# Kernel optimization log

Measured on AMD Instinct MI355X. Metric: run time of the kernel, lower is better.

Reference implementation:

```python
import jax, jax.numpy as jnp
import numpy as np

P = 16      # patch size
D = 768     # d_model
H = 12      # heads
L = 12      # layers
F = 3072    # d_ff
NC = 1000   # num classes
B = 32
IMG = 224
S = (IMG // P) ** 2 + 1  # 197 tokens (CLS + patches)
EPS = 1e-5


def layernorm(x, s, b):
    m = jnp.mean(x, axis=-1, keepdims=True)
    v = jnp.var(x, axis=-1, keepdims=True)
    return (x - m) * jax.lax.rsqrt(v + EPS) * s + b


def setup_inputs() -> dict:
    key = jax.random.key(0)
    ks = jax.random.split(key, 16)
    sd = 0.02
    patch_dim = P * P * 3  # 768
    inp = {
        "img": jax.random.normal(ks[0], (B, 3, IMG, IMG), jnp.float32),
        "proj_w": jax.random.normal(ks[1], (patch_dim, D), jnp.float32) * sd,
        "proj_b": jnp.zeros((D,), jnp.float32),
        "cls_token": jax.random.normal(ks[2], (1, 1, D), jnp.float32) * sd,
        "pos_emb": jax.random.normal(ks[3], (1, S, D), jnp.float32) * sd,
        # stacked per-layer params [L, ...]
        "ln1_s": jnp.ones((L, D), jnp.float32),
        "ln1_b": jnp.zeros((L, D), jnp.float32),
        "wq": jax.random.normal(ks[4], (L, D, D), jnp.float32) * sd,
        "bq": jnp.zeros((L, D), jnp.float32),
        "wk": jax.random.normal(ks[5], (L, D, D), jnp.float32) * sd,
        "bk": jnp.zeros((L, D), jnp.float32),
        "wv": jax.random.normal(ks[6], (L, D, D), jnp.float32) * sd,
        "bv": jnp.zeros((L, D), jnp.float32),
        "wo": jax.random.normal(ks[7], (L, D, D), jnp.float32) * sd,
        "bo": jnp.zeros((L, D), jnp.float32),
        "ln2_s": jnp.ones((L, D), jnp.float32),
        "ln2_b": jnp.zeros((L, D), jnp.float32),
        "w1": jax.random.normal(ks[8], (L, D, F), jnp.float32) * sd,
        "b1": jnp.zeros((L, F), jnp.float32),
        "w2": jax.random.normal(ks[9], (L, F, D), jnp.float32) * sd,
        "b2": jnp.zeros((L, D), jnp.float32),
        "fnorm_s": jnp.ones((D,), jnp.float32),
        "fnorm_b": jnp.zeros((D,), jnp.float32),
        "head_w": jax.random.normal(ks[10], (D, NC), jnp.float32) * sd,
        "head_b": jnp.zeros((NC,), jnp.float32),
    }
    return inp


def vit_forward(img, proj_w, proj_b, cls_token, pos_emb, ln1_s, ln1_b,
                wq, bq, wk, bk, wv, bv, wo, bo, ln2_s, ln2_b,
                w1, b1, w2, b2, fnorm_s, fnorm_b, head_w, head_b):
    b = img.shape[0]
    g = IMG // P
    # rearrange 'b c (h ph) (w pw) -> b (h w) (ph pw c)'
    x = img.reshape(b, 3, g, P, g, P)
    x = x.transpose(0, 2, 4, 3, 5, 1).reshape(b, g * g, P * P * 3)
    x = x @ proj_w + proj_b                      # [b, 196, D]
    cls = jnp.broadcast_to(cls_token, (b, 1, D))
    x = jnp.concatenate([cls, x], axis=1)        # [b, 197, D]
    x = x + pos_emb                              # learnable positional encoding

    dk = D // H
    scale = 1.0 / jnp.sqrt(jnp.float32(dk))

    def layer(x, p):
        (l1s, l1b, Wq, Bq, Wk, Bk, Wv, Bv, Wo, Bo,
         l2s, l2b, W1, B1, W2, B2) = p
        # pre-norm self-attention with residual
        xn = layernorm(x, l1s, l1b)
        q = (xn @ Wq + Bq).reshape(b, S, H, dk)
        k = (xn @ Wk + Bk).reshape(b, S, H, dk)
        v = (xn @ Wv + Bv).reshape(b, S, H, dk)
        scores = jnp.einsum('bqhd,bkhd->bhqk', q, k) * scale
        attn = jax.nn.softmax(scores, axis=-1)
        ao = jnp.einsum('bhqk,bkhd->bqhd', attn, v).reshape(b, S, D)
        x = x + (ao @ Wo + Bo)
        # pre-norm FFN with residual
        xn = layernorm(x, l2s, l2b)
        h = jax.nn.gelu(xn @ W1 + B1, approximate=False)
        x = x + (h @ W2 + B2)
        return x, None

    params = (ln1_s, ln1_b, wq, bq, wk, bk, wv, bv, wo, bo,
              ln2_s, ln2_b, w1, b1, w2, b2)
    x, _ = jax.lax.scan(layer, x, params)
    x = layernorm(x, fnorm_s, fnorm_b)
    cls_out = x[:, 0, :]
    return cls_out @ head_w + head_b             # [b, num_classes]


def reference(img, proj_w, proj_b, cls_token, pos_emb, ln1_s, ln1_b,
              wq, bq, wk, bk, wv, bv, wo, bo, ln2_s, ln2_b,
              w1, b1, w2, b2, fnorm_s, fnorm_b, head_w, head_b):
    return vit_forward(img, proj_w, proj_b, cls_token, pos_emb, ln1_s, ln1_b,
                       wq, bq, wk, bk, wv, bv, wo, bo, ln2_s, ln2_b,
                       w1, b1, w2, b2, fnorm_s, fnorm_b, head_w, head_b)
```

## Files before the change

kernel.cpp:

```cpp
#include <hip/hip_runtime.h>
#include <stdint.h>

typedef __attribute__((ext_vector_type(4))) float  f32x4;
typedef __attribute__((ext_vector_type(8))) _Float16 f16x8;
typedef __attribute__((ext_vector_type(8))) unsigned short u16x8;

__device__ __forceinline__ unsigned short f2h(float f) {
    _Float16 h = (_Float16)f;
    union { _Float16 h; unsigned short u; } cv; cv.h = h; return cv.u;
}

__device__ __forceinline__ f32x4 mfma16(f16x8 a, f16x8 b, f32x4 c) {
    return __builtin_amdgcn_mfma_f32_16x16x32_f16(a, b, c, 0, 0, 0);
}

__device__ __forceinline__ void async16(const unsigned short* g, unsigned short* l) {
    __builtin_amdgcn_global_load_lds(
        (const __attribute__((address_space(1))) unsigned int*)g,
        (__attribute__((address_space(3))) unsigned int*)l,
        16, 0, 0);
}

template<int EPI, int BK>
__global__ __launch_bounds__(256, (BK == 32 ? 4 : 3))
void gemm_k(const unsigned short* __restrict__ A, const unsigned short* __restrict__ Bw,
            int M, int K, int N,
            float* __restrict__ p0, unsigned short* __restrict__ p1,
            const float* __restrict__ p2, const float* __restrict__ p3,
            unsigned short* __restrict__ p4, unsigned short* __restrict__ p5)
{
    __shared__ unsigned short lA[2][64 * BK];
    __shared__ unsigned short lB[2][128 * BK];
    const int tid  = threadIdx.x;
    const int lane = tid & 63;
    const int wid  = tid >> 6;

    const int gx  = gridDim.x;
    const int nwg = gx * gridDim.y;
    const int lin = blockIdx.y * gx + blockIdx.x;
    const int q = nwg >> 3, r = nwg & 7;
    const int xcd = lin & 7, i = lin >> 3;
    const int wg  = (xcd < r ? xcd * (q + 1) : r * (q + 1) + (xcd - r) * q) + i;
    const int m0 = (wg / gx) * 64;
    const int n0 = (wg % gx) * 128;

    const int colBase = wid * 32;
    const int fr = lane & 15, fg = lane >> 4;

    f32x4 acc[4][2];
#pragma unroll
    for (int a = 0; a < 4; ++a)
#pragma unroll
        for (int b = 0; b < 2; ++b) acc[a][b] = (f32x4){0.f, 0.f, 0.f, 0.f};

    const int nk = K / BK;
    constexpr int CPR = BK / 8;
    constexpr int ACH = 64 * CPR;
    constexpr int NH  = (ACH + 128 * CPR) / 256;

    auto stage = [&](int buf, int kt) {
        const int k0 = kt * BK;
#pragma unroll
        for (int h = 0; h < NH; ++h) {
            const int c = h * 256 + tid;
            const int wbase = h * 256 + wid * 64;
            if (c < ACH) {
                const int row = c / CPR, kc = c % CPR;
                const int gkc = (BK == 32) ? (kc ^ ((row >> 1) & 3)) : (kc ^ (row & 7));
                int ar = m0 + row; if (ar > M - 1) ar = M - 1;
                async16(A + (size_t)ar * K + k0 + gkc * 8,
                        &lA[buf][(size_t)wbase * 8]);
            } else {
                const int cb = c - ACH;
                const int row = cb / CPR, kc = cb % CPR;
                const int gkc = (BK == 32) ? (kc ^ ((row >> 1) & 3)) : (kc ^ (row & 7));
                async16(Bw + (size_t)(n0 + row) * K + k0 + gkc * 8,
                        &lB[buf][(size_t)(wbase - ACH) * 8]);
            }
        }
    };

    stage(0, 0);
    for (int kt = 0; kt < nk; ++kt) {
        __syncthreads();
        if (kt + 1 < nk) stage((kt + 1) & 1, kt + 1);
        const int buf = kt & 1;
#pragma unroll
        for (int kk = 0; kk < BK / 32; ++kk) {
            f16x8 af[4], bfv[2];
#pragma unroll
            for (int mi = 0; mi < 4; ++mi) {
                int row = mi * 16 + fr;
                int pc  = (BK == 32) ? (fg ^ ((row >> 1) & 3))
                                     : ((kk * 4 + fg) ^ (row & 7));
                af[mi] = *(const f16x8*)(&lA[buf][row * BK + pc * 8]);
            }
#pragma unroll
            for (int ni = 0; ni < 2; ++ni) {
                int row = colBase + ni * 16 + fr;
                int pc  = (BK == 32) ? (fg ^ ((row >> 1) & 3))
                                     : ((kk * 4 + fg) ^ (row & 7));
                bfv[ni] = *(const f16x8*)(&lB[buf][row * BK + pc * 8]);
            }
#pragma unroll
            for (int mi = 0; mi < 4; ++mi)
#pragma unroll
                for (int ni = 0; ni < 2; ++ni)
                    acc[mi][ni] = mfma16(af[mi], bfv[ni], acc[mi][ni]);
        }
    }

#pragma unroll
    for (int mi = 0; mi < 4; ++mi) {
#pragma unroll
        for (int ni = 0; ni < 2; ++ni) {
            const int col = n0 + colBase + ni * 16 + fr;
#pragma unroll
            for (int reg = 0; reg < 4; ++reg) {
                const int row = m0 + mi * 16 + fg * 4 + reg;
                if (row >= M) continue;
                const float v = acc[mi][ni][reg];
                if constexpr (EPI == 0) {
                    int mat = col / 768;
                    int w   = col - mat * 768;
                    int h   = w >> 6, d = w & 63;
                    int b   = row / 197, s = row - b * 197;
                    float val = v + p2[col];
                    if (mat == 2) {
                        p5[(((size_t)b * 12 + h) * 64 + d) * 208 + s] = f2h(val);
                    } else {
                        unsigned short* dst = (mat == 0) ? p1 : p4;
                        dst[(((size_t)b * 12 + h) * 197 + s) * 64 + d] = f2h(val);
                    }
                } else if constexpr (EPI == 1 || EPI == 3) {
                    size_t idx = (size_t)row * 768 + col;
                    p0[idx] = p0[idx] + v + p2[col];
                } else if constexpr (EPI == 2) {
                    float val = v + p2[col];
                    float g = 0.5f * val * (1.0f + erff(val * 0.70710678118654752f));
                    p1[(size_t)row * 3072 + col] = f2h(g);
                } else {
                    int b = row / 196, p = row - b * 196;
                    float val = v + p2[col] + p3[(size_t)(1 + p) * 768 + col];
                    p0[((size_t)(b * 197 + 1 + p)) * 768 + col] = val;
                }
            }
        }
    }
}

__global__ __launch_bounds__(256, 4)
void attn_k(const unsigned short* __restrict__ qb, const unsigned short* __restrict__ kb,
            const unsigned short* __restrict__ vt, unsigned short* __restrict__ ao)
{
    __shared__ float sc[32 * 210];
    __shared__ float rinv[32];

    const int qt = blockIdx.x;
    const int bh = blockIdx.y;
    const int b = bh / 12, h = bh - b * 12;
    const unsigned short* qh  = qb + (size_t)bh * 197 * 64;
    const unsigned short* kh  = kb + (size_t)bh * 197 * 64;
    const unsigned short* vth = vt + (size_t)bh * 64 * 208;
    const int tid = threadIdx.x, lane = tid & 63, wid = tid >> 6;
    const int fr = lane & 15, fg = lane >> 4;

    f16x8 qf[2][2];
#pragma unroll
    for (int mi = 0; mi < 2; ++mi)
#pragma unroll
        for (int kc = 0; kc < 2; ++kc) {
            int s = qt * 32 + mi * 16 + fr; if (s > 196) s = 196;
            qf[mi][kc] = *(const f16x8*)(qh + (size_t)s * 64 + kc * 32 + fg * 8);
        }

    for (int nt = wid; nt < 13; nt += 4) {
        f32x4 a0 = (f32x4){0.f,0.f,0.f,0.f}, a1 = a0;
        int rs = nt * 16 + fr; if (rs > 196) rs = 196;
#pragma unroll
        for (int kc = 0; kc < 2; ++kc) {
            f16x8 kf = *(const f16x8*)(kh + (size_t)rs * 64 + kc * 32 + fg * 8);
            a0 = mfma16(qf[0][kc], kf, a0);
            a1 = mfma16(qf[1][kc], kf, a1);
        }
        int ccol = nt * 16 + fr;
        bool valid = (ccol < 197);
#pragma unroll
        for (int reg = 0; reg < 4; ++reg) {
            int mr = fg * 4 + reg;
            sc[mr * 210 + ccol]        = valid ? a0[reg] * 0.125f : -1e30f;
            sc[(16 + mr) * 210 + ccol] = valid ? a1[reg] * 0.125f : -1e30f;
        }
    }
    __syncthreads();

    {
        int row = tid >> 3, j = tid & 7;
        float m = -1e30f;
        for (int c = j; c < 208; c += 8) m = fmaxf(m, sc[row * 210 + c]);
#pragma unroll
        for (int o = 1; o < 8; o <<= 1) m = fmaxf(m, __shfl_xor(m, o));
        float sum = 0.f;
        for (int c = j; c < 208; c += 8) {
            float e = __expf(sc[row * 210 + c] - m);
            sc[row * 210 + c] = e;
            sum += e;
        }
#pragma unroll
        for (int o = 1; o < 8; o <<= 1) sum += __shfl_xor(sum, o);
        if (j == 0) rinv[row] = 1.0f / sum;
    }
    __syncthreads();

    f32x4 o0 = (f32x4){0.f,0.f,0.f,0.f}, o1 = o0;
    const int dbase = wid * 16;
    for (int kt = 0; kt < 7; ++kt) {
        int kb8 = kt * 32 + fg * 8;
        f16x8 pa0, pa1, vf;
        if (kb8 >= 208) {
#pragma unroll
            for (int j = 0; j < 8; ++j) { pa0[j] = (_Float16)0.f; pa1[j] = (_Float16)0.f; vf[j] = (_Float16)0.f; }
        } else {
            const float* pr0 = &sc[fr * 210 + kb8];
            const float* pr1 = &sc[(16 + fr) * 210 + kb8];
#pragma unroll
            for (int j = 0; j < 8; ++j) { pa0[j] = (_Float16)pr0[j]; pa1[j] = (_Float16)pr1[j]; }
            vf = *(const f16x8*)(vth + (size_t)(dbase + fr) * 208 + kb8);
        }
        o0 = mfma16(pa0, vf, o0);
        o1 = mfma16(pa1, vf, o1);
    }
#pragma unroll
    for (int reg = 0; reg < 4; ++reg) {
        int mr0 = fg * 4 + reg, s0 = qt * 32 + mr0;
        if (s0 < 197)
            ao[((size_t)(b * 197 + s0)) * 768 + h * 64 + dbase + fr] = f2h(o0[reg] * rinv[mr0]);
        int mr1 = 16 + fg * 4 + reg, s1 = qt * 32 + mr1;
        if (s1 < 197)
            ao[((size_t)(b * 197 + s1)) * 768 + h * 64 + dbase + fr] = f2h(o1[reg] * rinv[mr1]);
    }
}

__global__ __launch_bounds__(256, 4)
void ln_k(const float* __restrict__ x, const float* __restrict__ gs,
          const float* __restrict__ gb, unsigned short* __restrict__ out)
{
    const int row = blockIdx.x;
    const int tid = threadIdx.x, lane = tid & 63, wid = tid >> 6;
    const float* xr = x + (size_t)row * 768;
    float v0 = xr[tid], v1 = xr[tid + 256], v2 = xr[tid + 512];
    float s = v0 + v1 + v2;
    float q = v0 * v0 + v1 * v1 + v2 * v2;
#pragma unroll
    for (int o = 1; o < 64; o <<= 1) { s += __shfl_xor(s, o); q += __shfl_xor(q, o); }
    __shared__ float ws[4], wq[4];
    if (lane == 0) { ws[wid] = s; wq[wid] = q; }
    __syncthreads();
    s = ws[0] + ws[1] + ws[2] + ws[3];
    q = wq[0] + wq[1] + wq[2] + wq[3];
    const float mean = s * (1.0f / 768.0f);
    const float rstd = rsqrtf(q * (1.0f / 768.0f) - mean * mean + 1e-5f);
    unsigned short* orow = out + (size_t)row * 768;
    orow[tid]       = f2h((v0 - mean) * rstd * gs[tid]       + gb[tid]);
    orow[tid + 256] = f2h((v1 - mean) * rstd * gs[tid + 256] + gb[tid + 256]);
    orow[tid + 512] = f2h((v2 - mean) * rstd * gs[tid + 512] + gb[tid + 512]);
}

__device__ __forceinline__ void convT_dev(const float* __restrict__ src,
                                          unsigned short* __restrict__ dst,
                                          int K, int N, int bx, int by)
{
    __shared__ float t[64][65];
    const int tid = threadIdx.x;
    const int n0 = bx * 64, k0 = by * 64;
    int r = tid >> 4, cq = tid & 15;
#pragma unroll
    for (int i = 0; i < 4; ++i) {
        f32x4 v = *(const f32x4*)(src + (size_t)(k0 + r + i * 16) * N + n0 + cq * 4);
        t[r + i * 16][cq * 4 + 0] = v.x;
        t[r + i * 16][cq * 4 + 1] = v.y;
        t[r + i * 16][cq * 4 + 2] = v.z;
        t[r + i * 16][cq * 4 + 3] = v.w;
    }
    __syncthreads();
    int nl = tid >> 2, kq = tid & 3;
    u16x8 o0, o1;
#pragma unroll
    for (int j = 0; j < 8; ++j) {
        o0[j] = f2h(t[kq * 16 + j][nl]);
        o1[j] = f2h(t[kq * 16 + 8 + j][nl]);
    }
    unsigned short* d = dst + (size_t)(n0 + nl) * K + k0 + kq * 16;
    *(u16x8*)(d)     = o0;
    *(u16x8*)(d + 8) = o1;
}

__global__ __launch_bounds__(256)
void convT_k(const float* __restrict__ src, unsigned short* __restrict__ dst, int K, int N)
{
    convT_dev(src, dst, K, N, blockIdx.x, blockIdx.y);
}

__global__ __launch_bounds__(256)
void prep_k(const float* __restrict__ wq, const float* __restrict__ wk,
            const float* __restrict__ wv, const float* __restrict__ wo,
            const float* __restrict__ w1, const float* __restrict__ w2,
            const float* __restrict__ bq, const float* __restrict__ bk,
            const float* __restrict__ bv,
            unsigned short* __restrict__ wqkvT, unsigned short* __restrict__ woT,
            unsigned short* __restrict__ w1T, unsigned short* __restrict__ w2T,
            float* __restrict__ bqkv)
{
    const int bid = blockIdx.x;
    if (bid == 1728) {
        for (int c = threadIdx.x; c < 2304; c += 256) {
            int m = c / 768, w = c - m * 768;
            bqkv[c] = (m == 0) ? bq[w] : (m == 1 ? bk[w] : bv[w]);
        }
        return;
    }
    const float* src; unsigned short* dst; int K, N, bx, by;
    if (bid < 576) {
        int mat = bid / 144, r = bid - mat * 144;
        K = 768; N = 768; bx = r % 12; by = r / 12;
        if (mat == 0)      { src = wq; dst = wqkvT; }
        else if (mat == 1) { src = wk; dst = wqkvT + 768ull * 768; }
        else if (mat == 2) { src = wv; dst = wqkvT + 1536ull * 768; }
        else               { src = wo; dst = woT; }
    } else if (bid < 1152) {
        int r = bid - 576; K = 768; N = 3072; bx = r % 48; by = r / 48;
        src = w1; dst = w1T;
    } else {
        int r = bid - 1152; K = 3072; N = 768; bx = r % 12; by = r / 12;
        src = w2; dst = w2T;
    }
    convT_dev(src, dst, K, N, bx, by);
}

__global__ __launch_bounds__(256)
void patch_k(const float* __restrict__ img, unsigned short* __restrict__ patches)
{
    const int t = blockIdx.x;
    const int pxy = threadIdx.x;
    const int b = t / 196, pi = t - b * 196;
    const int gy = pi / 14, gx = pi - gy * 14;
    const int py = pxy >> 4, px = pxy & 15;
    const int yy = gy * 16 + py, xx = gx * 16 + px;
    const float* base = img + ((size_t)b * 3 * 224 + yy) * 224 + xx;
    float c0 = base[0];
    float c1 = base[224 * 224];
    float c2 = base[2 * 224 * 224];
    unsigned short* d = patches + (size_t)t * 768 + pxy * 3;
    d[0] = f2h(c0); d[1] = f2h(c1); d[2] = f2h(c2);
}

__global__ void cls_k(const float* __restrict__ cls, const float* __restrict__ pos,
                      float* __restrict__ x)
{
    int c = blockIdx.x * 256 + threadIdx.x;
    int b = blockIdx.y;
    x[((size_t)b * 197) * 768 + c] = cls[c] + pos[c];
}

__global__ __launch_bounds__(256, 4)
void head_k(const float* __restrict__ x, const float* __restrict__ fs, const float* __restrict__ fb,
            const float* __restrict__ hw, const float* __restrict__ hb, float* __restrict__ out)
{
    __shared__ float xn[768];
    __shared__ float ws[4], wq_[4];
    const int b  = blockIdx.y;
    const int n0 = blockIdx.x * 125;
    const int tid = threadIdx.x, lane = tid & 63, wid = tid >> 6;
    const float* xr = x + (size_t)b * 197 * 768;
    float v0 = xr[tid], v1 = xr[tid + 256], v2 = xr[tid + 512];
    float s = v0 + v1 + v2, q = v0 * v0 + v1 * v1 + v2 * v2;
#pragma unroll
    for (int o = 1; o < 64; o <<= 1) { s += __shfl_xor(s, o); q += __shfl_xor(q, o); }
    if (lane == 0) { ws[wid] = s; wq_[wid] = q; }
    __syncthreads();
    s = ws[0] + ws[1] + ws[2] + ws[3];
    q = wq_[0] + wq_[1] + wq_[2] + wq_[3];
    float mean = s * (1.f / 768.f);
    float rstd = rsqrtf(q * (1.f / 768.f) - mean * mean + 1e-5f);
    xn[tid]       = (v0 - mean) * rstd * fs[tid]       + fb[tid];
    xn[tid + 256] = (v1 - mean) * rstd * fs[tid + 256] + fb[tid + 256];
    xn[tid + 512] = (v2 - mean) * rstd * fs[tid + 512] + fb[tid + 512];
    __syncthreads();

    const int nrel = tid >> 1, half = tid & 1;
    const int n = n0 + nrel;
    float acc = 0.f;
    if (nrel < 125) {
        const float* hp = hw + (size_t)(half * 384) * 1000 + n;
        const float* xp = xn + half * 384;
#pragma unroll 4
        for (int k = 0; k < 384; ++k) acc = fmaf(xp[k], hp[(size_t)k * 1000], acc);
    }
    acc += __shfl_xor(acc, 1);
    if (half == 0 && nrel < 125) out[(size_t)b * 1000 + n] = acc + hb[n];
}

extern "C" void kernel_launch(void* const* d_in, const int* in_sizes, int n_in,
                              void* d_out, int out_size, void* d_ws, size_t ws_size,
                              hipStream_t stream)
{
    (void)in_sizes; (void)n_in; (void)out_size; (void)ws_size;
    const float* img    = (const float*)d_in[0];
    const float* proj_w = (const float*)d_in[1];
    const float* proj_b = (const float*)d_in[2];
    const float* cls_t  = (const float*)d_in[3];
    const float* pos    = (const float*)d_in[4];
    const float* ln1_s  = (const float*)d_in[5];
    const float* ln1_b  = (const float*)d_in[6];
    const float* wq     = (const float*)d_in[7];
    const float* bq     = (const float*)d_in[8];
    const float* wk     = (const float*)d_in[9];
    const float* bk     = (const float*)d_in[10];
    const float* wv     = (const float*)d_in[11];
    const float* bv     = (const float*)d_in[12];
    const float* wo     = (const float*)d_in[13];
    const float* bo     = (const float*)d_in[14];
    const float* ln2_s  = (const float*)d_in[15];
    const float* ln2_b  = (const float*)d_in[16];
    const float* w1     = (const float*)d_in[17];
    const float* b1     = (const float*)d_in[18];
    const float* w2     = (const float*)d_in[19];
    const float* b2     = (const float*)d_in[20];
    const float* fs     = (const float*)d_in[21];
    const float* fb     = (const float*)d_in[22];
    const float* hw     = (const float*)d_in[23];
    const float* hb     = (const float*)d_in[24];

    char* ws = (char*)d_ws;
    size_t off = 0;
    auto alloc = [&](size_t bytes) -> char* {
        char* r = ws + off;
        off += (bytes + 255) & ~(size_t)255;
        return r;
    };
    unsigned short* wqkvT = (unsigned short*)alloc(2304ull * 768 * 2);
    unsigned short* woT   = (unsigned short*)alloc(768ull * 768 * 2);
    unsigned short* w1T   = (unsigned short*)alloc(3072ull * 768 * 2);
    unsigned short* w2T   = (unsigned short*)alloc(768ull * 3072 * 2);
    float*          bqkv  = (float*)alloc(2304 * 4);
    unsigned short* projT = (unsigned short*)alloc(768ull * 768 * 2);
    float*          x     = (float*)alloc(6304ull * 768 * 4);
    unsigned short* xn    = (unsigned short*)alloc(6304ull * 768 * 2);
    unsigned short* qbuf  = (unsigned short*)alloc(4841472ull * 2);
    unsigned short* kbuf  = (unsigned short*)alloc(4841472ull * 2);
    unsigned short* vbufT = (unsigned short*)alloc(384ull * 64 * 208 * 2);
    unsigned short* aob   = (unsigned short*)alloc(6304ull * 768 * 2);
    unsigned short* hbuf  = (unsigned short*)alloc(6304ull * 3072 * 2);
    unsigned short* patches = hbuf;

    convT_k<<<dim3(12, 12), 256, 0, stream>>>(proj_w, projT, 768, 768);
    patch_k<<<dim3(6272), 256, 0, stream>>>(img, patches);
    gemm_k<4, 32><<<dim3(6, 98), 256, 0, stream>>>(patches, projT, 6272, 768, 768,
                                                   x, nullptr, proj_b, pos, nullptr, nullptr);
    cls_k<<<dim3(3, 32), 256, 0, stream>>>(cls_t, pos, x);

    for (int l = 0; l < 12; ++l) {
        prep_k<<<dim3(1729), 256, 0, stream>>>(
            wq + (size_t)l * 768 * 768, wk + (size_t)l * 768 * 768,
            wv + (size_t)l * 768 * 768, wo + (size_t)l * 768 * 768,
            w1 + (size_t)l * 768 * 3072, w2 + (size_t)l * 3072 * 768,
            bq + l * 768, bk + l * 768, bv + l * 768,
            wqkvT, woT, w1T, w2T, bqkv);

        ln_k<<<dim3(6304), 256, 0, stream>>>(x, ln1_s + l * 768, ln1_b + l * 768, xn);
        gemm_k<0, 32><<<dim3(18, 99), 256, 0, stream>>>(xn, wqkvT, 6304, 768, 2304,
                                                        nullptr, qbuf, bqkv, nullptr, kbuf, vbufT);
        attn_k<<<dim3(7, 384), 256, 0, stream>>>(qbuf, kbuf, vbufT, aob);
        gemm_k<1, 32><<<dim3(6, 99), 256, 0, stream>>>(aob, woT, 6304, 768, 768,
                                                       x, nullptr, bo + l * 768, nullptr, nullptr, nullptr);
        ln_k<<<dim3(6304), 256, 0, stream>>>(x, ln2_s + l * 768, ln2_b + l * 768, xn);
        gemm_k<2, 32><<<dim3(24, 99), 256, 0, stream>>>(xn, w1T, 6304, 768, 3072,
                                                        nullptr, hbuf, b1 + l * 3072, nullptr, nullptr, nullptr);
        gemm_k<3, 64><<<dim3(6, 99), 256, 0, stream>>>(hbuf, w2T, 6304, 3072, 768,
                                                       x, nullptr, b2 + l * 768, nullptr, nullptr, nullptr);
    }

    head_k<<<dim3(8, 32), 256, 0, stream>>>(x, fs, fb, hw, hb, (float*)d_out);
}
```

Measured before the change: 3.252 ms.

## Double-buffer weight prep and fuse next-layer prep into attention launch

Weight transpose/convert for layer l+1 now runs as extra blocks inside the attention kernel of layer l, using double-buffered weight buffers. Layer 0 prep is hoisted before the loop. This removes one kernel launch per layer and lets prep blocks fill idle CUs alongside attention work. The cost is twice the workspace for converted weights, and the prep blocks compete with attention for bandwidth and occupancy.

```diff
diff --git a/kernel.cpp b/kernel.cpp
--- a/kernel.cpp
+++ b/kernel.cpp
@@ -149,15 +149,112 @@
     }
 }
 
+__device__ __forceinline__ void convT_body(const float* __restrict__ src,
+                                           unsigned short* __restrict__ dst,
+                                           int K, int N, int bx, int by,
+                                           float (*t)[65])
+{
+    const int tid = threadIdx.x;
+    const int n0 = bx * 64, k0 = by * 64;
+    int r = tid >> 4, cq = tid & 15;
+#pragma unroll
+    for (int i = 0; i < 4; ++i) {
+        f32x4 v = *(const f32x4*)(src + (size_t)(k0 + r + i * 16) * N + n0 + cq * 4);
+        t[r + i * 16][cq * 4 + 0] = v.x;
+        t[r + i * 16][cq * 4 + 1] = v.y;
+        t[r + i * 16][cq * 4 + 2] = v.z;
+        t[r + i * 16][cq * 4 + 3] = v.w;
+    }
+    __syncthreads();
+    int nl = tid >> 2, kq = tid & 3;
+    u16x8 o0, o1;
+#pragma unroll
+    for (int j = 0; j < 8; ++j) {
+        o0[j] = f2h(t[kq * 16 + j][nl]);
+        o1[j] = f2h(t[kq * 16 + 8 + j][nl]);
+    }
+    unsigned short* d = dst + (size_t)(n0 + nl) * K + k0 + kq * 16;
+    *(u16x8*)(d)     = o0;
+    *(u16x8*)(d + 8) = o1;
+}
+
+__device__ __forceinline__ void prep_block(int pid,
+            const float* __restrict__ wq, const float* __restrict__ wk,
+            const float* __restrict__ wv, const float* __restrict__ wo,
+            const float* __restrict__ w1, const float* __restrict__ w2,
+            const float* __restrict__ bq, const float* __restrict__ bk,
+            const float* __restrict__ bv,
+            unsigned short* __restrict__ wqkvT, unsigned short* __restrict__ woT,
+            unsigned short* __restrict__ w1T, unsigned short* __restrict__ w2T,
+            float* __restrict__ bqkv, float (*t)[65])
+{
+    if (pid == 1728) {
+        for (int c = threadIdx.x; c < 2304; c += 256) {
+            int m = c / 768, w = c - m * 768;
+            bqkv[c] = (m == 0) ? bq[w] : (m == 1 ? bk[w] : bv[w]);
+        }
+        return;
+    }
+    const float* src; unsigned short* dst; int K, N, bx, by;
+    if (pid < 576) {
+        int mat = pid / 144, r = pid - mat * 144;
+        K = 768; N = 768; bx = r % 12; by = r / 12;
+        if (mat == 0)      { src = wq; dst = wqkvT; }
+        else if (mat == 1) { src = wk; dst = wqkvT + 768ull * 768; }
+        else if (mat == 2) { src = wv; dst = wqkvT + 1536ull * 768; }
+        else               { src = wo; dst = woT; }
+    } else if (pid < 1152) {
+        int r = pid - 576; K = 768; N = 3072; bx = r % 48; by = r / 48;
+        src = w1; dst = w1T;
+    } else {
+        int r = pid - 1152; K = 3072; N = 768; bx = r % 12; by = r / 12;
+        src = w2; dst = w2T;
+    }
+    convT_body(src, dst, K, N, bx, by, t);
+}
+
+__global__ __launch_bounds__(256)
+void prep_k(const float* __restrict__ wq, const float* __restrict__ wk,
+            const float* __restrict__ wv, const float* __restrict__ wo,
+            const float* __restrict__ w1, const float* __restrict__ w2,
+            const float* __restrict__ bq, const float* __restrict__ bk,
+            const float* __restrict__ bv,
+            unsigned short* __restrict__ wqkvT, unsigned short* __restrict__ woT,
+            unsigned short* __restrict__ w1T, unsigned short* __restrict__ w2T,
+            float* __restrict__ bqkv)
+{
+    __shared__ float t[64][65];
+    prep_block(blockIdx.x, wq, wk, wv, wo, w1, w2, bq, bk, bv,
+               wqkvT, woT, w1T, w2T, bqkv, t);
+}
+
 __global__ __launch_bounds__(256, 4)
-void attn_k(const unsigned short* __restrict__ qb, const unsigned short* __restrict__ kb,
-            const unsigned short* __restrict__ vt, unsigned short* __restrict__ ao)
-{
-    __shared__ float sc[32 * 210];
-    __shared__ float rinv[32];
-
-    const int qt = blockIdx.x;
-    const int bh = blockIdx.y;
+void attn_prep_k(const unsigned short* __restrict__ qb, const unsigned short* __restrict__ kb,
+                 const unsigned short* __restrict__ vt, unsigned short* __restrict__ ao,
+                 const float* __restrict__ wq, const float* __restrict__ wk,
+                 const float* __restrict__ wv, const float* __restrict__ wo,
+                 const float* __restrict__ w1, const float* __restrict__ w2,
+                 const float* __restrict__ bq, const float* __restrict__ bk,
+                 const float* __restrict__ bv,
+                 unsigned short* __restrict__ wqkvT, unsigned short* __restrict__ woT,
+                 unsigned short* __restrict__ w1T, unsigned short* __restrict__ w2T,
+                 float* __restrict__ bqkv)
+{
+    __shared__ float smbuf[32 * 210 + 32];
+
+    const int bid = blockIdx.x;
+    if (bid >= 2688) {
+        prep_block(bid - 2688, wq, wk, wv, wo, w1, w2, bq, bk, bv,
+                   wqkvT, woT, w1T, w2T, bqkv,
+                   reinterpret_cast<float(*)[65]>(smbuf));
+        return;
+    }
+
+    float* sc   = smbuf;
+    float* rinv = smbuf + 32 * 210;
+
+    const int bh = bid % 384;
+    const int qt = bid / 384;
     const int b = bh / 12, h = bh - b * 12;
     const unsigned short* qh  = qb + (size_t)bh * 197 * 64;
     const unsigned short* kh  = kb + (size_t)bh * 197 * 64;
@@ -266,75 +363,11 @@
     orow[tid + 512] = f2h((v2 - mean) * rstd * gs[tid + 512] + gb[tid + 512]);
 }
 
-__device__ __forceinline__ void convT_dev(const float* __restrict__ src,
-                                          unsigned short* __restrict__ dst,
-                                          int K, int N, int bx, int by)
-{
-    __shared__ float t[64][65];
-    const int tid = threadIdx.x;
-    const int n0 = bx * 64, k0 = by * 64;
-    int r = tid >> 4, cq = tid & 15;
-#pragma unroll
-    for (int i = 0; i < 4; ++i) {
-        f32x4 v = *(const f32x4*)(src + (size_t)(k0 + r + i * 16) * N + n0 + cq * 4);
-        t[r + i * 16][cq * 4 + 0] = v.x;
-        t[r + i * 16][cq * 4 + 1] = v.y;
-        t[r + i * 16][cq * 4 + 2] = v.z;
-        t[r + i * 16][cq * 4 + 3] = v.w;
-    }
-    __syncthreads();
-    int nl = tid >> 2, kq = tid & 3;
-    u16x8 o0, o1;
-#pragma unroll
-    for (int j = 0; j < 8; ++j) {
-        o0[j] = f2h(t[kq * 16 + j][nl]);
-        o1[j] = f2h(t[kq * 16 + 8 + j][nl]);
-    }
-    unsigned short* d = dst + (size_t)(n0 + nl) * K + k0 + kq * 16;
-    *(u16x8*)(d)     = o0;
-    *(u16x8*)(d + 8) = o1;
-}
-
 __global__ __launch_bounds__(256)
 void convT_k(const float* __restrict__ src, unsigned short* __restrict__ dst, int K, int N)
 {
-    convT_dev(src, dst, K, N, blockIdx.x, blockIdx.y);
-}
-
-__global__ __launch_bounds__(256)
-void prep_k(const float* __restrict__ wq, const float* __restrict__ wk,
-            const float* __restrict__ wv, const float* __restrict__ wo,
-            const float* __restrict__ w1, const float* __restrict__ w2,
-            const float* __restrict__ bq, const float* __restrict__ bk,
-            const float* __restrict__ bv,
-            unsigned short* __restrict__ wqkvT, unsigned short* __restrict__ woT,
-            unsigned short* __restrict__ w1T, unsigned short* __restrict__ w2T,
-            float* __restrict__ bqkv)
-{
-    const int bid = blockIdx.x;
-    if (bid == 1728) {
-        for (int c = threadIdx.x; c < 2304; c += 256) {
-            int m = c / 768, w = c - m * 768;
-            bqkv[c] = (m == 0) ? bq[w] : (m == 1 ? bk[w] : bv[w]);
-        }
-        return;
-    }
-    const float* src; unsigned short* dst; int K, N, bx, by;
-    if (bid < 576) {
-        int mat = bid / 144, r = bid - mat * 144;
-        K = 768; N = 768; bx = r % 12; by = r / 12;
-        if (mat == 0)      { src = wq; dst = wqkvT; }
-        else if (mat == 1) { src = wk; dst = wqkvT + 768ull * 768; }
-        else if (mat == 2) { src = wv; dst = wqkvT + 1536ull * 768; }
-        else               { src = wo; dst = woT; }
-    } else if (bid < 1152) {
-        int r = bid - 576; K = 768; N = 3072; bx = r % 48; by = r / 48;
-        src = w1; dst = w1T;
-    } else {
-        int r = bid - 1152; K = 3072; N = 768; bx = r % 12; by = r / 12;
-        src = w2; dst = w2T;
-    }
-    convT_dev(src, dst, K, N, bx, by);
+    __shared__ float t[64][65];
+    convT_body(src, dst, K, N, blockIdx.x, blockIdx.y, t);
 }
 
 __global__ __launch_bounds__(256)
@@ -438,11 +471,16 @@
         off += (bytes + 255) & ~(size_t)255;
         return r;
     };
-    unsigned short* wqkvT = (unsigned short*)alloc(2304ull * 768 * 2);
-    unsigned short* woT   = (unsigned short*)alloc(768ull * 768 * 2);
-    unsigned short* w1T   = (unsigned short*)alloc(3072ull * 768 * 2);
-    unsigned short* w2T   = (unsigned short*)alloc(768ull * 3072 * 2);
-    float*          bqkv  = (float*)alloc(2304 * 4);
+    unsigned short* wqkvT[2]; unsigned short* woT[2];
+    unsigned short* w1T[2];   unsigned short* w2T[2];
+    float* bqkv[2];
+    for (int s = 0; s < 2; ++s) {
+        wqkvT[s] = (unsigned short*)alloc(2304ull * 768 * 2);
+        woT[s]   = (unsigned short*)alloc(768ull * 768 * 2);
+        w1T[s]   = (unsigned short*)alloc(3072ull * 768 * 2);
+        w2T[s]   = (unsigned short*)alloc(768ull * 3072 * 2);
+        bqkv[s]  = (float*)alloc(2304 * 4);
+    }
     unsigned short* projT = (unsigned short*)alloc(768ull * 768 * 2);
     float*          x     = (float*)alloc(6304ull * 768 * 4);
     unsigned short* xn    = (unsigned short*)alloc(6304ull * 768 * 2);
@@ -455,28 +493,34 @@
 
     convT_k<<<dim3(12, 12), 256, 0, stream>>>(proj_w, projT, 768, 768);
     patch_k<<<dim3(6272), 256, 0, stream>>>(img, patches);
+    prep_k<<<dim3(1729), 256, 0, stream>>>(
+        wq, wk, wv, wo, w1, w2, bq, bk, bv,
+        wqkvT[0], woT[0], w1T[0], w2T[0], bqkv[0]);
     gemm_k<4, 32><<<dim3(6, 98), 256, 0, stream>>>(patches, projT, 6272, 768, 768,
                                                    x, nullptr, proj_b, pos, nullptr, nullptr);
     cls_k<<<dim3(3, 32), 256, 0, stream>>>(cls_t, pos, x);
 
     for (int l = 0; l < 12; ++l) {
-        prep_k<<<dim3(1729), 256, 0, stream>>>(
-            wq + (size_t)l * 768 * 768, wk + (size_t)l * 768 * 768,
-            wv + (size_t)l * 768 * 768, wo + (size_t)l * 768 * 768,
-            w1 + (size_t)l * 768 * 3072, w2 + (size_t)l * 3072 * 768,
-            bq + l * 768, bk + l * 768, bv + l * 768,
-            wqkvT, woT, w1T, w2T, bqkv);
+        const int set = l & 1, nxt = set ^ 1;
+        const int lp  = (l < 11) ? l + 1 : 11;
+        const int nprep = (l < 11) ? 1729 : 0;
 
         ln_k<<<dim3(6304), 256, 0, stream>>>(x, ln1_s + l * 768, ln1_b + l * 768, xn);
-        gemm_k<0, 32><<<dim3(18, 99), 256, 0, stream>>>(xn, wqkvT, 6304, 768, 2304,
-                                                        nullptr, qbuf, bqkv, nullptr, kbuf, vbufT);
-        attn_k<<<dim3(7, 384), 256, 0, stream>>>(qbuf, kbuf, vbufT, aob);
-        gemm_k<1, 32><<<dim3(6, 99), 256, 0, stream>>>(aob, woT, 6304, 768, 768,
+        gemm_k<0, 32><<<dim3(18, 99), 256, 0, stream>>>(xn, wqkvT[set], 6304, 768, 2304,
+                                                        nullptr, qbuf, bqkv[set], nullptr, kbuf, vbufT);
+        attn_prep_k<<<dim3(2688 + nprep), 256, 0, stream>>>(
+            qbuf, kbuf, vbufT, aob,
+            wq + (size_t)lp * 768 * 768, wk + (size_t)lp * 768 * 768,
+            wv + (size_t)lp * 768 * 768, wo + (size_t)lp * 768 * 768,
+            w1 + (size_t)lp * 768 * 3072, w2 + (size_t)lp * 3072 * 768,
+            bq + lp * 768, bk + lp * 768, bv + lp * 768,
+            wqkvT[nxt], woT[nxt], w1T[nxt], w2T[nxt], bqkv[nxt]);
+        gemm_k<1, 32><<<dim3(6, 99), 256, 0, stream>>>(aob, woT[set], 6304, 768, 768,
                                                        x, nullptr, bo + l * 768, nullptr, nullptr, nullptr);
         ln_k<<<dim3(6304), 256, 0, stream>>>(x, ln2_s + l * 768, ln2_b + l * 768, xn);
-        gemm_k<2, 32><<<dim3(24, 99), 256, 0, stream>>>(xn, w1T, 6304, 768, 3072,
+        gemm_k<2, 32><<<dim3(24, 99), 256, 0, stream>>>(xn, w1T[set], 6304, 768, 3072,
                                                         nullptr, hbuf, b1 + l * 3072, nullptr, nullptr, nullptr);
-        gemm_k<3, 64><<<dim3(6, 99), 256, 0, stream>>>(hbuf, w2T, 6304, 3072, 768,
+        gemm_k<3, 64><<<dim3(6, 99), 256, 0, stream>>>(hbuf, w2T[set], 6304, 3072, 768,
                                                        x, nullptr, b2 + l * 768, nullptr, nullptr, nullptr);
     }
 
```

Result: faster. 3.157 ms (-2.9%).
